# Kernel optimization log

Hardware: AMD Instinct MI355X
Metric: run time of the kernel (lower is better)

Reference implementation:

```python
import jax, jax.numpy as jnp
import numpy as np

N_NODES = 50000
N_EDGES = 800000
D_FEAT = 128
HIDDEN = 128
OUT = 128


def setup_inputs() -> dict:
    key = jax.random.key(0)
    ks = jax.random.split(key, 8)
    sc_in = 1.0 / np.sqrt(D_FEAT)
    sc_h = 1.0 / np.sqrt(HIDDEN)
    return {
        "x": jax.random.normal(ks[0], (N_NODES, D_FEAT), dtype=jnp.float32),
        "edge_index": jax.random.randint(ks[1], (2, N_EDGES), 0, N_NODES, dtype=jnp.int64),
        "W1_l": jax.random.normal(ks[2], (D_FEAT, HIDDEN), dtype=jnp.float32) * sc_in,
        "b1_l": jnp.zeros((HIDDEN,), dtype=jnp.float32),
        "W1_r": jax.random.normal(ks[3], (D_FEAT, HIDDEN), dtype=jnp.float32) * sc_in,
        "W2_l": jax.random.normal(ks[4], (HIDDEN, OUT), dtype=jnp.float32) * sc_h,
        "b2_l": jnp.zeros((OUT,), dtype=jnp.float32),
        "W2_r": jax.random.normal(ks[5], (HIDDEN, OUT), dtype=jnp.float32) * sc_h,
    }


def _sage_conv(x, src, dst, W_l, b_l, W_r, n_nodes):
    # mean aggregation of source features onto destination nodes
    msgs = x[src]  # [E, d] irregular gather
    summed = jax.ops.segment_sum(msgs, dst, num_segments=n_nodes)
    cnt = jax.ops.segment_sum(jnp.ones((src.shape[0],), x.dtype), dst, num_segments=n_nodes)
    aggr = summed / jnp.maximum(cnt, 1.0)[:, None]  # empty neighborhoods -> 0
    # PyG SAGEConv: lin_l(aggr) + lin_r(x_root); bias lives on lin_l
    return aggr @ W_l + b_l + x @ W_r


def reference(x, edge_index, W1_l, b1_l, W1_r, W2_l, b2_l, W2_r):
    src, dst = edge_index[0], edge_index[1]
    n = x.shape[0]
    h = _sage_conv(x, src, dst, W1_l, b1_l, W1_r, n)
    h = jax.nn.relu(h)
    out = _sage_conv(h, src, dst, W2_l, b2_l, W2_r, n)
    return out
```

## Files before the change

### kernel.cpp

```cpp
#include <hip/hip_runtime.h>

#define NN 50000
#define NE 800000
#define D 128
#define SEGBITS 8
#define SEGSZ 256
#define NSEG 196
#define GRID_A 512
#define EPB ((NE + GRID_A - 1) / GRID_A)
#define FLAT (NSEG * GRID_A)
#define SBLK ((FLAT + 255) / 256)

typedef __attribute__((ext_vector_type(8))) short short8;
typedef __attribute__((ext_vector_type(4))) float f32x4;

__device__ inline unsigned short f2bf(float f) {
    unsigned u = __builtin_bit_cast(unsigned, f);
    unsigned r = (u + 0x7fffu + ((u >> 16) & 1u)) >> 16;
    return (unsigned short)r;
}
__device__ inline float bflo(unsigned u) { return __builtin_bit_cast(float, u << 16); }
__device__ inline float bfhi(unsigned u) { return __builtin_bit_cast(float, u & 0xffff0000u); }


__global__ __launch_bounds__(256) void histA_kernel(const int* __restrict__ dst,
        int* __restrict__ bh) {
    __shared__ int h[NSEG];
    int t = threadIdx.x;
    if (t < NSEG) h[t] = 0;
    __syncthreads();
    int beg = blockIdx.x * EPB;
    int end = min(beg + EPB, NE);
    for (int e = beg + t; e < end; e += 256) atomicAdd(&h[dst[e] >> SEGBITS], 1);
    __syncthreads();
    if (t < NSEG) bh[t * GRID_A + blockIdx.x] = h[t];
}

__global__ __launch_bounds__(256) void partialS_kernel(const int* __restrict__ bh,
        int* __restrict__ bsum) {
    __shared__ int s[256];
    int t = threadIdx.x;
    int i = blockIdx.x * 256 + t;
    s[t] = (i < FLAT) ? bh[i] : 0;
    __syncthreads();
    #pragma unroll
    for (int off = 128; off > 0; off >>= 1) {
        if (t < off) s[t] += s[t + off];
        __syncthreads();
    }
    if (t == 0) bsum[blockIdx.x] = s[0];
}

__global__ __launch_bounds__(512) void scanS_kernel(const int* __restrict__ bsum,
        int* __restrict__ boff) {
    __shared__ int s[512];
    int t = threadIdx.x;
    int v = (t < SBLK) ? bsum[t] : 0;
    s[t] = v;
    __syncthreads();
    #pragma unroll
    for (int off = 1; off < 512; off <<= 1) {
        int u = (t >= off) ? s[t - off] : 0;
        __syncthreads();
        s[t] += u;
        __syncthreads();
    }
    if (t < SBLK) boff[t] = s[t] - v;
}

__global__ __launch_bounds__(256) void scan2S_kernel(const int* __restrict__ bh,
        const int* __restrict__ boff, int* __restrict__ bases,
        int* __restrict__ segBase) {
    __shared__ int s[256];
    int t = threadIdx.x;
    int i = blockIdx.x * 256 + t;
    int v = (i < FLAT) ? bh[i] : 0;
    s[t] = v;
    __syncthreads();
    #pragma unroll
    for (int off = 1; off < 256; off <<= 1) {
        int u = (t >= off) ? s[t - off] : 0;
        __syncthreads();
        s[t] += u;
        __syncthreads();
    }
    if (i < FLAT) {
        int excl = s[t] - v + boff[blockIdx.x];
        bases[i] = excl;
        if ((i & (GRID_A - 1)) == 0) segBase[i >> 9] = excl;
    }
    if (i == 0) segBase[NSEG] = NE;
}

__global__ __launch_bounds__(256) void scatA_kernel(const int* __restrict__ src,
        const int* __restrict__ dst, const int* __restrict__ bases,
        unsigned* __restrict__ bucket) {
    __shared__ int cur[NSEG];
    int t = threadIdx.x;
    if (t < NSEG) cur[t] = bases[t * GRID_A + blockIdx.x];
    __syncthreads();
    int beg = blockIdx.x * EPB;
    int end = min(beg + EPB, NE);
    for (int e = beg + t; e < end; e += 256) {
        int d = dst[e];
        int sg = d >> SEGBITS;
        int p = atomicAdd(&cur[sg], 1);
        bucket[p] = ((unsigned)(d & (SEGSZ - 1)) << 24) | (unsigned)src[e];
    }
}

__global__ __launch_bounds__(256) void buildB_kernel(const unsigned* __restrict__ bucket,
        const int* __restrict__ segBase, int* __restrict__ rowptr, int* __restrict__ csr) {
    __shared__ int h[SEGSZ];
    __shared__ int s[SEGSZ];
    int sg = blockIdx.x;
    int t = threadIdx.x;
    int beg = segBase[sg], end = segBase[sg + 1];
    h[t] = 0;
    __syncthreads();
    for (int i = beg + t; i < end; i += 256) atomicAdd(&h[bucket[i] >> 24], 1);
    __syncthreads();
    int v = h[t];
    s[t] = v;
    __syncthreads();
    #pragma unroll
    for (int off = 1; off < 256; off <<= 1) {
        int u = (t >= off) ? s[t - off] : 0;
        __syncthreads();
        s[t] += u;
        __syncthreads();
    }
    int excl = beg + s[t] - v;
    int n = sg * SEGSZ + t;
    if (n <= NN) rowptr[n] = excl;
    h[t] = excl;
    __syncthreads();
    for (int i = beg + t; i < end; i += 256) {
        unsigned u = bucket[i];
        int p = atomicAdd(&h[u >> 24], 1);
        csr[p] = (int)(u & 0xFFFFFFu);
    }
}


__global__ __launch_bounds__(256) void prep_w_kernel(const float* __restrict__ W0,
        const float* __restrict__ W1, const float* __restrict__ W2,
        const float* __restrict__ W3, unsigned short* __restrict__ O) {
    int t = blockIdx.x * 256 + threadIdx.x;
    int w = t >> 11;
    int rem = t & 2047;
    int f = rem >> 6, l = rem & 63;
    int ct = f >> 2, kk = f & 3;
    int col = ct * 16 + (l & 15);
    int k0 = kk * 32 + (l >> 4) * 8;
    const float* W = (w == 0) ? W0 : (w == 1) ? W1 : (w == 2) ? W2 : W3;
    unsigned short* o = O + (size_t)w * 16384 + ((size_t)f * 64 + l) * 8;
    #pragma unroll
    for (int e = 0; e < 8; ++e) o[e] = f2bf(W[(k0 + e) * D + col]);
}


template<int AFP32>
__global__ __launch_bounds__(256, 1) void gemm_kernel(const void* __restrict__ Av,
        const unsigned short* __restrict__ WfL, const unsigned short* __restrict__ WfR,
        unsigned short* __restrict__ Yb, unsigned short* __restrict__ Zb, int nrows) {
    __shared__ short8 sW[4096];

    for (int i = threadIdx.x; i < 2048; i += 256) {
        sW[i]        = ((const short8*)WfL)[i];
        sW[i + 2048] = ((const short8*)WfR)[i];
    }
    __syncthreads();

    int wv = threadIdx.x >> 6, l = threadIdx.x & 63;
    int r15 = l & 15, kg = l >> 4;
    int row0 = blockIdx.x * 128 + wv * 32;

    short8 a[2][4];
    #pragma unroll
    for (int rt = 0; rt < 2; ++rt) {
        #pragma unroll
        for (int kk = 0; kk < 4; ++kk) {
            int row = row0 + rt * 16 + r15;
            row = min(row, nrows - 1);
            int off = kk * 32 + kg * 8;
            if (AFP32) {
                const float* A = (const float*)Av;
                float4 p = *(const float4*)(A + (size_t)row * D + off);
                float4 q = *(const float4*)(A + (size_t)row * D + off + 4);
                short8 v;
                v[0] = (short)f2bf(p.x); v[1] = (short)f2bf(p.y);
                v[2] = (short)f2bf(p.z); v[3] = (short)f2bf(p.w);
                v[4] = (short)f2bf(q.x); v[5] = (short)f2bf(q.y);
                v[6] = (short)f2bf(q.z); v[7] = (short)f2bf(q.w);
                a[rt][kk] = v;
            } else {
                const unsigned short* A = (const unsigned short*)Av;
                a[rt][kk] = *(const short8*)(A + (size_t)row * D + off);
            }
        }
    }

    f32x4 accY[2][8] = {};
    f32x4 accZ[2][8] = {};
    #pragma unroll
    for (int ct = 0; ct < 8; ++ct) {
        #pragma unroll
        for (int kk = 0; kk < 4; ++kk) {
            short8 bL = sW[(ct * 4 + kk) * 64 + l];
            short8 bR = sW[2048 + (ct * 4 + kk) * 64 + l];
            accY[0][ct] = __builtin_amdgcn_mfma_f32_16x16x32_bf16(a[0][kk], bL, accY[0][ct], 0, 0, 0);
            accY[1][ct] = __builtin_amdgcn_mfma_f32_16x16x32_bf16(a[1][kk], bL, accY[1][ct], 0, 0, 0);
            accZ[0][ct] = __builtin_amdgcn_mfma_f32_16x16x32_bf16(a[0][kk], bR, accZ[0][ct], 0, 0, 0);
            accZ[1][ct] = __builtin_amdgcn_mfma_f32_16x16x32_bf16(a[1][kk], bR, accZ[1][ct], 0, 0, 0);
        }
    }

    #pragma unroll
    for (int rt = 0; rt < 2; ++rt) {
        #pragma unroll
        for (int ct = 0; ct < 8; ++ct) {
            #pragma unroll
            for (int i = 0; i < 4; ++i) {
                int row = row0 + rt * 16 + kg * 4 + i;
                if (row < nrows) {
                    int col = ct * 16 + r15;
                    Yb[(size_t)row * D + col] = f2bf(accY[rt][ct][i]);
                    Zb[(size_t)row * D + col] = f2bf(accZ[rt][ct][i]);
                }
            }
        }
    }
}


template<int RELU, int OUTBF16>
__global__ __launch_bounds__(256) void agg_ep_kernel(const unsigned short* __restrict__ Yb,
        const unsigned short* __restrict__ Zb, const float* __restrict__ bias,
        const int* __restrict__ rowptr, const int* __restrict__ csr,
        void* __restrict__ outp) {
    int lane = threadIdx.x & 63;
    int sub = lane >> 4;
    int m = lane & 15;
    int wv = (blockIdx.x << 2) + (threadIdx.x >> 6);
    int nw = gridDim.x << 2;
    float bb[8];
    #pragma unroll
    for (int e = 0; e < 8; ++e) bb[e] = bias[m * 8 + e];

    for (int node = wv; node < NN; node += nw) {
        int beg = rowptr[node], end = rowptr[node + 1];
        float acc[8] = {};
        for (int j = beg + sub; j < end; j += 4) {
            int sn = csr[j];
            uint4 u = *(const uint4*)(Yb + (size_t)sn * D + m * 8);
            acc[0] += bflo(u.x); acc[1] += bfhi(u.x);
            acc[2] += bflo(u.y); acc[3] += bfhi(u.y);
            acc[4] += bflo(u.z); acc[5] += bfhi(u.z);
            acc[6] += bflo(u.w); acc[7] += bfhi(u.w);
        }
        #pragma unroll
        for (int e = 0; e < 8; ++e) {
            acc[e] += __shfl_xor(acc[e], 16, 64);
            acc[e] += __shfl_xor(acc[e], 32, 64);
        }
        if (sub == 0) {
            float inv = (end > beg) ? 1.f / (float)(end - beg) : 0.f;
            uint4 uz = *(const uint4*)(Zb + (size_t)node * D + m * 8);
            float v[8];
            v[0] = acc[0] * inv + bb[0] + bflo(uz.x);
            v[1] = acc[1] * inv + bb[1] + bfhi(uz.x);
            v[2] = acc[2] * inv + bb[2] + bflo(uz.y);
            v[3] = acc[3] * inv + bb[3] + bfhi(uz.y);
            v[4] = acc[4] * inv + bb[4] + bflo(uz.z);
            v[5] = acc[5] * inv + bb[5] + bfhi(uz.z);
            v[6] = acc[6] * inv + bb[6] + bflo(uz.w);
            v[7] = acc[7] * inv + bb[7] + bfhi(uz.w);
            if (RELU) {
                #pragma unroll
                for (int e = 0; e < 8; ++e) v[e] = fmaxf(v[e], 0.f);
            }
            if (OUTBF16) {
                uint4 o;
                o.x = (unsigned)f2bf(v[0]) | ((unsigned)f2bf(v[1]) << 16);
                o.y = (unsigned)f2bf(v[2]) | ((unsigned)f2bf(v[3]) << 16);
                o.z = (unsigned)f2bf(v[4]) | ((unsigned)f2bf(v[5]) << 16);
                o.w = (unsigned)f2bf(v[6]) | ((unsigned)f2bf(v[7]) << 16);
                *(uint4*)((unsigned short*)outp + (size_t)node * D + m * 8) = o;
            } else {
                float* op = (float*)outp + (size_t)node * D + m * 8;
                float4 o1 = {v[0], v[1], v[2], v[3]};
                float4 o2 = {v[4], v[5], v[6], v[7]};
                *(float4*)op = o1;
                *(float4*)(op + 4) = o2;
            }
        }
    }
}


extern "C" void kernel_launch(void* const* d_in, const int* in_sizes, int n_in,
                              void* d_out, int out_size, void* d_ws, size_t ws_size,
                              hipStream_t stream) {
    const float* x   = (const float*)d_in[0];
    const int*   ei  = (const int*)d_in[1];
    const float* W1l = (const float*)d_in[2];
    const float* b1  = (const float*)d_in[3];
    const float* W1r = (const float*)d_in[4];
    const float* W2l = (const float*)d_in[5];
    const float* b2  = (const float*)d_in[6];
    const float* W2r = (const float*)d_in[7];
    float* out = (float*)d_out;

    const int N = NN, E = NE;
    const int* src = ei;
    const int* dst = ei + E;

    char* ws = (char*)d_ws;
    size_t off = 0;
    auto alloc = [&](size_t bytes) -> void* {
        void* p = ws + off;
        off += (bytes + 255) & ~(size_t)255;
        return p;
    };
    int* rowptr  = (int*)alloc((size_t)(N + 1) * 4);
    int* csr     = (int*)alloc((size_t)E * 4);
    int* bh      = (int*)alloc((size_t)FLAT * 4);
    int* bases   = (int*)alloc((size_t)FLAT * 4);
    int* bsumS   = (int*)alloc((size_t)SBLK * 4);
    int* boffS   = (int*)alloc((size_t)SBLK * 4);
    int* segBase = (int*)alloc((size_t)(NSEG + 1) * 4);
    unsigned* bucket = (unsigned*)alloc((size_t)E * 4);
    unsigned short* hb  = (unsigned short*)alloc((size_t)N * D * 2);
    unsigned short* Yb  = (unsigned short*)alloc((size_t)N * D * 2);
    unsigned short* Zb  = (unsigned short*)alloc((size_t)N * D * 2);
    unsigned short* wf  = (unsigned short*)alloc((size_t)4 * 16384 * 2);

    histA_kernel<<<GRID_A, 256, 0, stream>>>(dst, bh);
    partialS_kernel<<<SBLK, 256, 0, stream>>>(bh, bsumS);
    scanS_kernel<<<1, 512, 0, stream>>>(bsumS, boffS);
    scan2S_kernel<<<SBLK, 256, 0, stream>>>(bh, boffS, bases, segBase);
    scatA_kernel<<<GRID_A, 256, 0, stream>>>(src, dst, bases, bucket);
    buildB_kernel<<<NSEG, 256, 0, stream>>>(bucket, segBase, rowptr, csr);

    prep_w_kernel<<<32, 256, 0, stream>>>(W1l, W1r, W2l, W2r, wf);

    unsigned short* wf1l = wf;
    unsigned short* wf1r = wf + 16384;
    unsigned short* wf2l = wf + 2 * 16384;
    unsigned short* wf2r = wf + 3 * 16384;

    int gblocks = (N + 127) / 128;

    gemm_kernel<1><<<gblocks, 256, 0, stream>>>(x, wf1l, wf1r, Yb, Zb, N);
    agg_ep_kernel<1, 1><<<2048, 256, 0, stream>>>(Yb, Zb, b1, rowptr, csr, hb);

    gemm_kernel<0><<<gblocks, 256, 0, stream>>>(hb, wf2l, wf2r, Yb, Zb, N);
    agg_ep_kernel<0, 0><<<2048, 256, 0, stream>>>(Yb, Zb, b2, rowptr, csr, out);
}
```

Before: 139.9 us.

## Fuse weight prep into histogram, widen bucket grid, unroll gather loop

Folds the weight-conversion work into the first histogram kernel so one launch is dropped. Doubles the number of blocks used for histogramming and scattering edges, resizing the scan kernels to match. Unrolls the neighbour gather loop by two so each lane has two row loads in flight, and makes the final fp32 output stores nontemporal. More blocks raise parallelism in the CSR build but enlarge the histogram table that must be scanned.

```diff
diff --git a/kernel.cpp b/kernel.cpp
--- a/kernel.cpp
+++ b/kernel.cpp
@@ -6,7 +6,7 @@
 #define SEGBITS 8
 #define SEGSZ 256
 #define NSEG 196
-#define GRID_A 512
+#define GRID_A 1024
 #define EPB ((NE + GRID_A - 1) / GRID_A)
 #define FLAT (NSEG * GRID_A)
 #define SBLK ((FLAT + 255) / 256)
@@ -24,16 +24,32 @@
 
 
 __global__ __launch_bounds__(256) void histA_kernel(const int* __restrict__ dst,
-        int* __restrict__ bh) {
+        int* __restrict__ bh,
+        const float* __restrict__ W0, const float* __restrict__ W1,
+        const float* __restrict__ W2, const float* __restrict__ W3,
+        unsigned short* __restrict__ wf) {
     __shared__ int h[NSEG];
     int t = threadIdx.x;
+    int b = blockIdx.x;
     if (t < NSEG) h[t] = 0;
     __syncthreads();
-    int beg = blockIdx.x * EPB;
+    int beg = b * EPB;
     int end = min(beg + EPB, NE);
     for (int e = beg + t; e < end; e += 256) atomicAdd(&h[dst[e] >> SEGBITS], 1);
     __syncthreads();
-    if (t < NSEG) bh[t * GRID_A + blockIdx.x] = h[t];
+    if (t < NSEG) bh[t * GRID_A + b] = h[t];
+    if (b < 32) {
+        int tg = b * 256 + t;
+        int w = tg >> 11, rem = tg & 2047;
+        int f = rem >> 6, l = rem & 63;
+        int ct = f >> 2, kk = f & 3;
+        int col = ct * 16 + (l & 15);
+        int k0 = kk * 32 + (l >> 4) * 8;
+        const float* W = (w == 0) ? W0 : (w == 1) ? W1 : (w == 2) ? W2 : W3;
+        unsigned short* o = wf + (size_t)w * 16384 + ((size_t)f * 64 + l) * 8;
+        #pragma unroll
+        for (int e = 0; e < 8; ++e) o[e] = f2bf(W[(k0 + e) * D + col]);
+    }
 }
 
 __global__ __launch_bounds__(256) void partialS_kernel(const int* __restrict__ bh,
@@ -51,15 +67,15 @@
     if (t == 0) bsum[blockIdx.x] = s[0];
 }
 
-__global__ __launch_bounds__(512) void scanS_kernel(const int* __restrict__ bsum,
+__global__ __launch_bounds__(1024) void scanS_kernel(const int* __restrict__ bsum,
         int* __restrict__ boff) {
-    __shared__ int s[512];
+    __shared__ int s[1024];
     int t = threadIdx.x;
     int v = (t < SBLK) ? bsum[t] : 0;
     s[t] = v;
     __syncthreads();
     #pragma unroll
-    for (int off = 1; off < 512; off <<= 1) {
+    for (int off = 1; off < 1024; off <<= 1) {
         int u = (t >= off) ? s[t - off] : 0;
         __syncthreads();
         s[t] += u;
@@ -87,7 +103,7 @@
     if (i < FLAT) {
         int excl = s[t] - v + boff[blockIdx.x];
         bases[i] = excl;
-        if ((i & (GRID_A - 1)) == 0) segBase[i >> 9] = excl;
+        if ((i & (GRID_A - 1)) == 0) segBase[i >> 10] = excl;
     }
     if (i == 0) segBase[NSEG] = NE;
 }
@@ -140,23 +156,6 @@
         int p = atomicAdd(&h[u >> 24], 1);
         csr[p] = (int)(u & 0xFFFFFFu);
     }
-}
-
-
-__global__ __launch_bounds__(256) void prep_w_kernel(const float* __restrict__ W0,
-        const float* __restrict__ W1, const float* __restrict__ W2,
-        const float* __restrict__ W3, unsigned short* __restrict__ O) {
-    int t = blockIdx.x * 256 + threadIdx.x;
-    int w = t >> 11;
-    int rem = t & 2047;
-    int f = rem >> 6, l = rem & 63;
-    int ct = f >> 2, kk = f & 3;
-    int col = ct * 16 + (l & 15);
-    int k0 = kk * 32 + (l >> 4) * 8;
-    const float* W = (w == 0) ? W0 : (w == 1) ? W1 : (w == 2) ? W2 : W3;
-    unsigned short* o = O + (size_t)w * 16384 + ((size_t)f * 64 + l) * 8;
-    #pragma unroll
-    for (int e = 0; e < 8; ++e) o[e] = f2bf(W[(k0 + e) * D + col]);
 }
 
 
@@ -251,13 +250,28 @@
     for (int node = wv; node < NN; node += nw) {
         int beg = rowptr[node], end = rowptr[node + 1];
         float acc[8] = {};
-        for (int j = beg + sub; j < end; j += 4) {
-            int sn = csr[j];
-            uint4 u = *(const uint4*)(Yb + (size_t)sn * D + m * 8);
-            acc[0] += bflo(u.x); acc[1] += bfhi(u.x);
-            acc[2] += bflo(u.y); acc[3] += bfhi(u.y);
-            acc[4] += bflo(u.z); acc[5] += bfhi(u.z);
-            acc[6] += bflo(u.w); acc[7] += bfhi(u.w);
+        int j = beg + sub;
+        for (; j + 4 < end; j += 8) {
+            int sa = csr[j];
+            int sb = csr[j + 4];
+            uint4 ua = *(const uint4*)(Yb + (size_t)sa * D + m * 8);
+            uint4 ub = *(const uint4*)(Yb + (size_t)sb * D + m * 8);
+            acc[0] += bflo(ua.x); acc[1] += bfhi(ua.x);
+            acc[2] += bflo(ua.y); acc[3] += bfhi(ua.y);
+            acc[4] += bflo(ua.z); acc[5] += bfhi(ua.z);
+            acc[6] += bflo(ua.w); acc[7] += bfhi(ua.w);
+            acc[0] += bflo(ub.x); acc[1] += bfhi(ub.x);
+            acc[2] += bflo(ub.y); acc[3] += bfhi(ub.y);
+            acc[4] += bflo(ub.z); acc[5] += bfhi(ub.z);
+            acc[6] += bflo(ub.w); acc[7] += bfhi(ub.w);
+        }
+        if (j < end) {
+            int sa = csr[j];
+            uint4 ua = *(const uint4*)(Yb + (size_t)sa * D + m * 8);
+            acc[0] += bflo(ua.x); acc[1] += bfhi(ua.x);
+            acc[2] += bflo(ua.y); acc[3] += bfhi(ua.y);
+            acc[4] += bflo(ua.z); acc[5] += bfhi(ua.z);
+            acc[6] += bflo(ua.w); acc[7] += bfhi(ua.w);
         }
         #pragma unroll
         for (int e = 0; e < 8; ++e) {
@@ -289,10 +303,10 @@
                 *(uint4*)((unsigned short*)outp + (size_t)node * D + m * 8) = o;
             } else {
                 float* op = (float*)outp + (size_t)node * D + m * 8;
-                float4 o1 = {v[0], v[1], v[2], v[3]};
-                float4 o2 = {v[4], v[5], v[6], v[7]};
-                *(float4*)op = o1;
-                *(float4*)(op + 4) = o2;
+                f32x4 o1 = {v[0], v[1], v[2], v[3]};
+                f32x4 o2 = {v[4], v[5], v[6], v[7]};
+                __builtin_nontemporal_store(o1, (f32x4*)op);
+                __builtin_nontemporal_store(o2, (f32x4*)(op + 4));
             }
         }
     }
@@ -336,14 +350,12 @@
     unsigned short* Zb  = (unsigned short*)alloc((size_t)N * D * 2);
     unsigned short* wf  = (unsigned short*)alloc((size_t)4 * 16384 * 2);
 
-    histA_kernel<<<GRID_A, 256, 0, stream>>>(dst, bh);
+    histA_kernel<<<GRID_A, 256, 0, stream>>>(dst, bh, W1l, W1r, W2l, W2r, wf);
     partialS_kernel<<<SBLK, 256, 0, stream>>>(bh, bsumS);
-    scanS_kernel<<<1, 512, 0, stream>>>(bsumS, boffS);
+    scanS_kernel<<<1, 1024, 0, stream>>>(bsumS, boffS);
     scan2S_kernel<<<SBLK, 256, 0, stream>>>(bh, boffS, bases, segBase);
     scatA_kernel<<<GRID_A, 256, 0, stream>>>(src, dst, bases, bucket);
     buildB_kernel<<<NSEG, 256, 0, stream>>>(bucket, segBase, rowptr, csr);
-
-    prep_w_kernel<<<32, 256, 0, stream>>>(W1l, W1r, W2l, W2r, wf);
 
     unsigned short* wf1l = wf;
     unsigned short* wf1r = wf + 16384;
```

Result: faster. 132.6 us (-5.2%).
